# Performance work log

Hardware: AMD Instinct MI355X
Metric: run time of the kernel (lower is better)

## Reference

```python
import jax, jax.numpy as jnp
import numpy as np

N_NODES = 100000
N_EDGES = 1600000
D_IN = 64
D_HID = 64


def setup_inputs() -> dict:
    key = jax.random.key(0)
    ks = jax.random.split(key, 9)
    feat = jax.random.uniform(ks[0], (N_NODES, D_IN), dtype=jnp.float32) + 1e-3
    edge_index = jax.random.randint(ks[1], (2, N_EDGES), 0, N_NODES, dtype=jnp.int64)
    edge_vals = jax.random.uniform(ks[2], (N_EDGES,), dtype=jnp.float32) + 1e-3
    W1 = jax.random.normal(ks[3], (D_IN, D_HID), dtype=jnp.float32) * 0.1
    b1 = jax.random.normal(ks[4], (D_HID,), dtype=jnp.float32) * 0.1
    W2 = jax.random.normal(ks[5], (D_HID, D_HID), dtype=jnp.float32) * 0.1
    b2 = jax.random.normal(ks[6], (D_HID,), dtype=jnp.float32) * 0.1
    W3 = jax.random.normal(ks[7], (D_HID, 1), dtype=jnp.float32) * 0.1
    b3 = jax.random.normal(ks[8], (1,), dtype=jnp.float32) * 0.1
    return {"feat": feat, "edge_index": edge_index, "edge_vals": edge_vals,
            "W1": W1, "b1": b1, "W2": W2, "b2": b2, "W3": W3, "b3": b3}


def reference(feat, edge_index, edge_vals, W1, b1, W2, b2, W3, b3):
    N = feat.shape[0]
    src = edge_index[0]
    dst = edge_index[1]
    # --- __init__: A_hat = D^{-1} A D^{-1}, D = diag(row sums of A) ---
    deg_row = jax.ops.segment_sum(edge_vals, src, num_segments=N)
    deg_row = jnp.where(deg_row > 0, deg_row, 1.0)  # guard isolated nodes
    w_hat = edge_vals / (deg_row[src] * deg_row[dst])  # A_hat edge weights
    # --- GCNConv gcn_norm: add self loops (weight 1), symmetric D^{-1/2} norm ---
    loops = jnp.arange(N, dtype=src.dtype)
    row = jnp.concatenate([src, loops])   # message sources
    col = jnp.concatenate([dst, loops])   # message targets (aggregation index)
    w = jnp.concatenate([w_hat, jnp.ones((N,), dtype=feat.dtype)])
    deg = jax.ops.segment_sum(w, col, num_segments=N)
    dinv = jnp.where(deg > 0, jax.lax.rsqrt(deg), 0.0)
    norm = dinv[row] * w * dinv[col]      # [E+N]

    def gcn_conv(x, W, b):
        h = x @ W                          # [N, d_out]
        msg = norm[:, None] * h[row]       # gather + scale, [E+N, d_out]
        return jax.ops.segment_sum(msg, col, num_segments=N) + b

    # --- forward ---
    x = feat / jnp.sum(feat, axis=1, keepdims=True)
    x = jax.nn.relu(gcn_conv(x, W1, b1))
    x = jax.nn.relu(gcn_conv(x, W2, b2))
    x = gcn_conv(x, W3, b3)               # final layer, no activation
    return x
```

## Files before the change

kernel.cpp:

```cpp
#include <hip/hip_runtime.h>
#include <hip/hip_fp16.h>


#define CAP    48
#define NRL    256
#define NBMX   512
#define P0E    2048

#define PG     2048

__device__ __forceinline__ float dec_ev(unsigned pk) {
    return __half2float(__ushort_as_half((unsigned short)(pk >> 17)));
}
__device__ __forceinline__ float dec_ev15(unsigned pk) {
    return __half2float(__ushort_as_half((unsigned short)(pk & 0x7FFF)));
}

__global__ __launch_bounds__(256) void k_scatter(
        const int* __restrict__ src, const int* __restrict__ dst,
        const float* __restrict__ ev,
        int* __restrict__ meta_d, int2* __restrict__ part_blk,
        int* __restrict__ meta_s, int* __restrict__ parts_src,
        int E, int NB) {
    __shared__ int2 srt[P0E];
    __shared__ int  srs[P0E];
    __shared__ int hd[NBMX], cbd[NBMX], lod[NBMX];
    __shared__ int hs[NBMX], cbs[NBMX], los[NBMX];
    int bx = (int)blockIdx.x, tid = (int)threadIdx.x;
    int e0 = bx * P0E;
    int ne = E - e0; if (ne > P0E) ne = P0E; if (ne < 0) ne = 0;
    for (int i = tid; i < NB; i += 256) { hd[i] = 0; hs[i] = 0; }
    __syncthreads();
    for (int i = tid; i < ne; i += 256) {
        atomicAdd(&hd[dst[e0 + i] >> 8], 1);
        atomicAdd(&hs[src[e0 + i] >> 8], 1);
    }
    __syncthreads();
    int wv = tid >> 6, ln = tid & 63;
    if (wv < 2) {
        int* h  = wv ? hs  : hd;
        int* cb = wv ? cbs : cbd;
        int run = 0;
        #pragma unroll
        for (int k = 0; k < NBMX / 64; k++) {
            int idx = k * 64 + ln;
            int v = (idx < NB) ? h[idx] : 0;
            int sc = v;
            #pragma unroll
            for (int o = 1; o < 64; o <<= 1) {
                int u = __shfl_up(sc, o, 64);
                if (ln >= o) sc += u;
            }
            if (idx < NB) cb[idx] = run + sc - v;
            run += __shfl(sc, 63, 64);
        }
    }
    __syncthreads();
    for (int c = tid; c < NB; c += 256) {
        lod[c] = cbd[c];
        los[c] = cbs[c];
        meta_d[(size_t)bx * NB + c] = (cbd[c] << 16) | hd[c];
        meta_s[(size_t)bx * NB + c] = (cbs[c] << 16) | hs[c];
    }
    __syncthreads();
    for (int i = tid; i < ne; i += 256) {
        int e = e0 + i;
        int s = src[e], d = dst[e];
        float v = ev[e];
        unsigned evh = (unsigned)__half_as_ushort(__float2half_rn(v)) & 0x7FFF;
        int p = atomicAdd(&lod[d >> 8], 1);
        int2 r;
        r.x = ((d & (NRL - 1)) << 17) | s;
        r.y = __float_as_int(v);
        srt[p] = r;
        int q = atomicAdd(&los[s >> 8], 1);
        srs[q] = (int)(((unsigned)(s & (NRL - 1)) << 15) | evh);
    }
    __syncthreads();
    for (int i = tid; i < ne; i += 256) {
        part_blk[(size_t)bx * P0E + i]  = srt[i];
        parts_src[(size_t)bx * P0E + i] = srs[i];
    }
}

__global__ __launch_bounds__(256) void k_degacc(
        const int* __restrict__ parts_src, const int* __restrict__ meta_s,
        float* __restrict__ deg_row, int N, int NB, int nsb) {
    __shared__ float dl[NRL];
    int b = (int)blockIdx.x, tid = (int)threadIdx.x;
    if (tid < NRL) dl[tid] = 0.f;
    __syncthreads();
    for (int bx = tid; bx < nsb; bx += 256) {
        int m = meta_s[(size_t)bx * NB + b];
        int base = m >> 16, len = m & 0xFFFF;
        const int* seg = parts_src + (size_t)bx * P0E + base;
        for (int j = 0; j < len; j++) {
            unsigned pk = (unsigned)seg[j];
            atomicAdd(&dl[pk >> 15], dec_ev15(pk));
        }
    }
    __syncthreads();
    int node = (b << 8) + tid;
    if (tid < NRL && node < N) deg_row[node] = dl[tid];
}

__global__ __launch_bounds__(256) void k_gemm1(
        const float* __restrict__ feat, const float* __restrict__ W1,
        __half* __restrict__ B, int N) {
    int lane = threadIdx.x & 63;
    float w[64];
    #pragma unroll
    for (int k = 0; k < 64; k++) w[k] = W1[k * 64 + lane];
    int wid = (int)blockIdx.x * 4 + (threadIdx.x >> 6);
    const int nw = PG * 4;
    for (int node = wid; node < N; node += nw) {
        float v = feat[(size_t)node * 64 + lane];
        float s = v;
        #pragma unroll
        for (int o = 1; o < 64; o <<= 1) s += __shfl_xor(s, o, 64);
        int myb = __float_as_int(v / s);
        float a0 = 0.f, a1 = 0.f, a2 = 0.f, a3 = 0.f;
        #pragma unroll
        for (int k = 0; k < 64; k += 4) {
            a0 = fmaf(__int_as_float(__builtin_amdgcn_readlane(myb, k + 0)), w[k + 0], a0);
            a1 = fmaf(__int_as_float(__builtin_amdgcn_readlane(myb, k + 1)), w[k + 1], a1);
            a2 = fmaf(__int_as_float(__builtin_amdgcn_readlane(myb, k + 2)), w[k + 2], a2);
            a3 = fmaf(__int_as_float(__builtin_amdgcn_readlane(myb, k + 3)), w[k + 3], a3);
        }
        B[(size_t)node * 64 + lane] = __float2half((a0 + a1) + (a2 + a3));
    }
}

__global__ __launch_bounds__(256) void k_bucket(
        const int2* __restrict__ part_blk, const int* __restrict__ meta_d,
        const float* __restrict__ deg_row,
        int* __restrict__ cnt, int* __restrict__ epair,
        float* __restrict__ di_t, float* __restrict__ r_t,
        int N, int NB, int nsb) {
    __shared__ int   lbuck[NRL * CAP];
    __shared__ int   lcnt[NRL];
    __shared__ float lt[NRL];
    int b = (int)blockIdx.x, tid = (int)threadIdx.x;
    if (tid < NRL) { lcnt[tid] = 0; lt[tid] = 0.f; }
    __syncthreads();
    for (int bx = tid; bx < nsb; bx += 256) {
        int m = meta_d[(size_t)bx * NB + b];
        int base = m >> 16, len = m & 0xFFFF;
        const int2* seg = part_blk + (size_t)bx * P0E + base;
        for (int j = 0; j < len; j++) {
            int2 r = seg[j];
            int dl = (r.x >> 17) & (NRL - 1);
            int s  = r.x & 0x1FFFF;
            float v = __int_as_float(r.y);
            atomicAdd(&lt[dl], v / deg_row[s]);
            unsigned evh = (unsigned)__half_as_ushort(__float2half_rn(v)) & 0x7FFF;
            int p = atomicAdd(&lcnt[dl], 1);
            if (p < CAP) lbuck[dl * CAP + p] = (int)((evh << 17) | (unsigned)s);
        }
    }
    __syncthreads();
    int node0 = b << 8;
    if (tid < NRL) {
        int node = node0 + tid;
        if (node < N) {
            int c = lcnt[tid]; if (c > CAP) c = CAP;
            cnt[node] = c;
            float drd = deg_row[node];
            drd = drd > 0.f ? drd : 1.f;
            float qd = 1.0f / drd;
            float di = rsqrtf(1.0f + qd * lt[tid]);
            di_t[node] = di;
            r_t[node]  = qd * di;
        }
    }
    __syncthreads();
    size_t base = (size_t)node0 * CAP;
    for (int i = tid; i < NRL * CAP; i += 256) epair[base + i] = lbuck[i];
}

__global__ __launch_bounds__(256) void k_p3(const int* __restrict__ cnt,
                                            int* __restrict__ epair,
                                            const float* __restrict__ r_t, int N) {
    int lane = threadIdx.x & 63;
    int node = blockIdx.x * 4 + (threadIdx.x >> 6);
    if (node >= N) return;
    int c = cnt[node]; if (c > CAP) c = CAP;
    if (lane < c) {
        size_t o = (size_t)node * CAP + lane;
        unsigned e = (unsigned)epair[o];
        int s = (int)(e & 0x1FFFF);
        float w = dec_ev(e) * r_t[s];
        unsigned wh = (unsigned)__half_as_ushort(__float2half_rn(w)) & 0x7FFF;
        epair[o] = (int)((wh << 17) | (unsigned)s);
    }
}

__device__ __forceinline__ float gather_rl(int c, int rec,
        const __half* __restrict__ h, int lane) {
    float a0 = 0.f, a1 = 0.f, a2 = 0.f, a3 = 0.f;
    int k = 0;
    for (; k + 16 <= c; k += 16) {
        int e[16]; float hv[16];
        #pragma unroll
        for (int j = 0; j < 16; j++) e[j] = __builtin_amdgcn_readlane(rec, k + j);
        #pragma unroll
        for (int j = 0; j < 16; j++)
            hv[j] = __half2float(h[(size_t)(e[j] & 0x1FFFF) * 64 + lane]);
        #pragma unroll
        for (int j = 0; j < 16; j++) {
            float wv = dec_ev((unsigned)e[j]);
            if ((j & 3) == 0)      a0 = fmaf(wv, hv[j], a0);
            else if ((j & 3) == 1) a1 = fmaf(wv, hv[j], a1);
            else if ((j & 3) == 2) a2 = fmaf(wv, hv[j], a2);
            else                   a3 = fmaf(wv, hv[j], a3);
        }
    }
    for (; k + 8 <= c; k += 8) {
        int e0 = __builtin_amdgcn_readlane(rec, k + 0);
        int e1 = __builtin_amdgcn_readlane(rec, k + 1);
        int e2 = __builtin_amdgcn_readlane(rec, k + 2);
        int e3 = __builtin_amdgcn_readlane(rec, k + 3);
        int e4 = __builtin_amdgcn_readlane(rec, k + 4);
        int e5 = __builtin_amdgcn_readlane(rec, k + 5);
        int e6 = __builtin_amdgcn_readlane(rec, k + 6);
        int e7 = __builtin_amdgcn_readlane(rec, k + 7);
        float h0 = __half2float(h[(size_t)(e0 & 0x1FFFF) * 64 + lane]);
        float h1 = __half2float(h[(size_t)(e1 & 0x1FFFF) * 64 + lane]);
        float h2 = __half2float(h[(size_t)(e2 & 0x1FFFF) * 64 + lane]);
        float h3 = __half2float(h[(size_t)(e3 & 0x1FFFF) * 64 + lane]);
        float h4 = __half2float(h[(size_t)(e4 & 0x1FFFF) * 64 + lane]);
        float h5 = __half2float(h[(size_t)(e5 & 0x1FFFF) * 64 + lane]);
        float h6 = __half2float(h[(size_t)(e6 & 0x1FFFF) * 64 + lane]);
        float h7 = __half2float(h[(size_t)(e7 & 0x1FFFF) * 64 + lane]);
        a0 = fmaf(dec_ev((unsigned)e0), h0, a0);
        a1 = fmaf(dec_ev((unsigned)e1), h1, a1);
        a2 = fmaf(dec_ev((unsigned)e2), h2, a2);
        a3 = fmaf(dec_ev((unsigned)e3), h3, a3);
        a0 = fmaf(dec_ev((unsigned)e4), h4, a0);
        a1 = fmaf(dec_ev((unsigned)e5), h5, a1);
        a2 = fmaf(dec_ev((unsigned)e6), h6, a2);
        a3 = fmaf(dec_ev((unsigned)e7), h7, a3);
    }
    for (; k + 4 <= c; k += 4) {
        int e0 = __builtin_amdgcn_readlane(rec, k + 0);
        int e1 = __builtin_amdgcn_readlane(rec, k + 1);
        int e2 = __builtin_amdgcn_readlane(rec, k + 2);
        int e3 = __builtin_amdgcn_readlane(rec, k + 3);
        float h0 = __half2float(h[(size_t)(e0 & 0x1FFFF) * 64 + lane]);
        float h1 = __half2float(h[(size_t)(e1 & 0x1FFFF) * 64 + lane]);
        float h2 = __half2float(h[(size_t)(e2 & 0x1FFFF) * 64 + lane]);
        float h3 = __half2float(h[(size_t)(e3 & 0x1FFFF) * 64 + lane]);
        a0 = fmaf(dec_ev((unsigned)e0), h0, a0);
        a1 = fmaf(dec_ev((unsigned)e1), h1, a1);
        a2 = fmaf(dec_ev((unsigned)e2), h2, a2);
        a3 = fmaf(dec_ev((unsigned)e3), h3, a3);
    }
    for (; k < c; k++) {
        int e0 = __builtin_amdgcn_readlane(rec, k);
        a0 = fmaf(dec_ev((unsigned)e0),
                  __half2float(h[(size_t)(e0 & 0x1FFFF) * 64 + lane]), a0);
    }
    return (a0 + a1) + (a2 + a3);
}

__global__ __launch_bounds__(256) void k_gath1(
        const int* __restrict__ cnt, const int* __restrict__ epair,
        const __half* __restrict__ B,
        const float* __restrict__ di_t, const float* __restrict__ r_t,
        const float* __restrict__ b1, __half* __restrict__ X2, int N) {
    int lane = threadIdx.x & 63;
    int node = (int)blockIdx.x * 4 + (threadIdx.x >> 6);
    if (node >= N) return;
    int un = __builtin_amdgcn_readfirstlane(node);
    int c  = __builtin_amdgcn_readfirstlane(cnt[un]);
    if (c > CAP) c = CAP;
    int rec = 0;
    if (lane < c) rec = epair[(size_t)un * CAP + lane];
    float own = __half2float(B[(size_t)un * 64 + lane]);
    float g   = gather_rl(c, rec, B, lane);
    float di  = di_t[un], rd = r_t[un];
    float x2  = fmaxf(b1[lane] + di * di * own + rd * g, 0.f);
    X2[(size_t)un * 64 + lane] = __float2half(x2);
}

__global__ __launch_bounds__(256) void k_gemm2(
        const __half* __restrict__ X2, const float* __restrict__ W2,
        __half* __restrict__ C, int N) {
    int lane = threadIdx.x & 63;
    float w[64];
    #pragma unroll
    for (int k = 0; k < 64; k++) w[k] = W2[k * 64 + lane];
    int wid = (int)blockIdx.x * 4 + (threadIdx.x >> 6);
    const int nw = PG * 4;
    for (int node = wid; node < N; node += nw) {
        int myb = __float_as_int(__half2float(X2[(size_t)node * 64 + lane]));
        float a0 = 0.f, a1 = 0.f, a2 = 0.f, a3 = 0.f;
        #pragma unroll
        for (int k = 0; k < 64; k += 4) {
            a0 = fmaf(__int_as_float(__builtin_amdgcn_readlane(myb, k + 0)), w[k + 0], a0);
            a1 = fmaf(__int_as_float(__builtin_amdgcn_readlane(myb, k + 1)), w[k + 1], a1);
            a2 = fmaf(__int_as_float(__builtin_amdgcn_readlane(myb, k + 2)), w[k + 2], a2);
            a3 = fmaf(__int_as_float(__builtin_amdgcn_readlane(myb, k + 3)), w[k + 3], a3);
        }
        C[(size_t)node * 64 + lane] = __float2half((a0 + a1) + (a2 + a3));
    }
}

__global__ __launch_bounds__(256) void k_gather_dot(
        const int* __restrict__ cnt, const int* __restrict__ epair,
        const __half* __restrict__ C,
        const float* __restrict__ di_t, const float* __restrict__ r_t,
        const float* __restrict__ b2, const float* __restrict__ W3,
        float* __restrict__ h3, int N) {
    int lane = threadIdx.x & 63;
    int node = (int)blockIdx.x * 4 + (threadIdx.x >> 6);
    if (node >= N) return;
    int un = __builtin_amdgcn_readfirstlane(node);
    int c  = __builtin_amdgcn_readfirstlane(cnt[un]);
    if (c > CAP) c = CAP;
    int rec = 0;
    if (lane < c) rec = epair[(size_t)un * CAP + lane];
    float own = __half2float(C[(size_t)un * 64 + lane]);
    float g   = gather_rl(c, rec, C, lane);
    float di  = di_t[un], rd = r_t[un];
    float p   = fmaxf(b2[lane] + di * di * own + rd * g, 0.f) * W3[lane];
    #pragma unroll
    for (int o = 1; o < 64; o <<= 1) p += __shfl_xor(p, o, 64);
    if (lane == 0) h3[un] = p;
}

__global__ __launch_bounds__(256) void k_gather1(const int* __restrict__ cnt,
                                                 const int* __restrict__ epair,
                                                 const float* __restrict__ h3,
                                                 const float* __restrict__ di_t,
                                                 const float* __restrict__ r_t,
                                                 const float* __restrict__ b3,
                                                 float* __restrict__ out, int N) {
    int lane = threadIdx.x & 63;
    int node = blockIdx.x * 4 + (threadIdx.x >> 6);
    if (node >= N) return;
    int c = cnt[node]; if (c > CAP) c = CAP;
    float e0 = 0.f;
    if (lane < c) {
        unsigned pk = (unsigned)epair[(size_t)node * CAP + lane];
        e0 = dec_ev(pk) * h3[pk & 0x1FFFF];
    }
    #pragma unroll
    for (int o = 1; o < 64; o <<= 1) e0 += __shfl_xor(e0, o, 64);
    if (lane == 0) {
        float di = di_t[node];
        out[node] = b3[0] + di * di * h3[node] + r_t[node] * e0;
    }
}

extern "C" void kernel_launch(void* const* d_in, const int* in_sizes, int n_in,
                              void* d_out, int out_size, void* d_ws, size_t ws_size,
                              hipStream_t stream) {
    const float* feat = (const float*)d_in[0];
    const int*   eidx = (const int*)d_in[1];
    const float* ev   = (const float*)d_in[2];
    const float* W1 = (const float*)d_in[3];
    const float* b1 = (const float*)d_in[4];
    const float* W2 = (const float*)d_in[5];
    const float* b2 = (const float*)d_in[6];
    const float* W3 = (const float*)d_in[7];
    const float* b3 = (const float*)d_in[8];

    const int N = in_sizes[0] / 64;
    const int E = in_sizes[2];
    const int* src = eidx;
    const int* dst = eidx + E;
    const int NB   = (N + NRL - 1) / NRL;
    const int npad = NB * NRL;
    const int nsb  = (E + P0E - 1) / P0E;

    char* p = (char*)d_ws;
    auto carve = [&](size_t nbytes) { char* r = p; p += (nbytes + 255) & ~(size_t)255; return r; };
    float*    deg_row   = (float*)   carve((size_t)N * 4);
    float*    di_t      = (float*)   carve((size_t)N * 4);
    float*    r_t       = (float*)   carve((size_t)N * 4);
    float*    h3        = (float*)   carve((size_t)N * 4);
    int*      cnt       = (int*)     carve((size_t)npad * 4);
    int*      meta_d    = (int*)     carve((size_t)nsb * NB * 4);
    int*      meta_s    = (int*)     carve((size_t)nsb * NB * 4);
    int*      epair     = (int*)     carve((size_t)npad * CAP * 4);
    int2*     part_blk  = (int2*)    carve((size_t)nsb * P0E * 8);
    int*      parts_src = (int*)     carve((size_t)nsb * P0E * 4);
    __half*   B         = (__half*)  carve((size_t)N * 64 * 2);
    __half*   X2        = (__half*)part_blk;
    __half*   C         = (__half*)B;
    float*    out       = (float*)d_out;

    const int BLK = 256;
    int gNode4 = (N + 3) / 4;

    k_scatter   <<<nsb, BLK, 0, stream>>>(src, dst, ev, meta_d, part_blk,
                                          meta_s, parts_src, E, NB);
    k_degacc    <<<NB, BLK, 0, stream>>>(parts_src, meta_s, deg_row, N, NB, nsb);
    k_gemm1     <<<PG, BLK, 0, stream>>>(feat, W1, B, N);
    k_bucket    <<<NB, BLK, 0, stream>>>(part_blk, meta_d, deg_row, cnt, epair,
                                         di_t, r_t, N, NB, nsb);
    k_p3        <<<gNode4, BLK, 0, stream>>>(cnt, epair, r_t, N);

    k_gath1     <<<gNode4, BLK, 0, stream>>>(cnt, epair, B, di_t, r_t, b1, X2, N);
    k_gemm2     <<<PG, BLK, 0, stream>>>(X2, W2, C, N);
    k_gather_dot<<<gNode4, BLK, 0, stream>>>(cnt, epair, C, di_t, r_t,
                                             b2, W3, h3, N);
    k_gather1   <<<gNode4, BLK, 0, stream>>>(cnt, epair, h3, di_t, r_t, b3, out, N);
}
```

Before: 330.5 us.

## Gather 8 neighbor rows per wave with 16-byte vector loads

Replaces the per-lane scalar half loads in the neighbor gather with a scheme where the wave is split into 8 groups of 8 lanes. Each group fetches a different neighbor's 128-byte feature row using uint4 loads, accumulates 8 features per lane, and then reduces across groups with xor shuffles. This aims to cut the number of memory instructions and increase memory-level parallelism on the random-access gather. In exchange it adds a cross-group shuffle reduction, leaves partially idle lanes when degree is not a multiple of 8, and changes the order of float accumulation.

```diff
diff --git a/kernel.cpp b/kernel.cpp
--- a/kernel.cpp
+++ b/kernel.cpp
@@ -195,72 +195,49 @@
     }
 }
 
-__device__ __forceinline__ float gather_rl(int c, int rec,
-        const __half* __restrict__ h, int lane) {
-    float a0 = 0.f, a1 = 0.f, a2 = 0.f, a3 = 0.f;
-    int k = 0;
-    for (; k + 16 <= c; k += 16) {
-        int e[16]; float hv[16];
+__device__ __forceinline__ void gather8(int c, int rec,
+        const __half* __restrict__ h, int grp, int sub, float acc[8]) {
+    #pragma unroll
+    for (int q = 0; q < 8; q++) acc[q] = 0.f;
+    int nb = (c + 7) >> 3;
+    for (int t = 0; t < nb; t += 2) {
+        int r0 = __shfl(rec, (t << 3) + grp, 64);
+        int s0 = r0 & 0x1FFFF;
+        float w0 = dec_ev((unsigned)r0);
+        uint4 d0 = *reinterpret_cast<const uint4*>(h + ((size_t)s0 << 6) + (sub << 3));
+        bool have1 = (t + 1 < nb);
+        uint4 d1; float w1 = 0.f;
+        if (have1) {
+            int r1 = __shfl(rec, (t << 3) + 8 + grp, 64);
+            int s1 = r1 & 0x1FFFF;
+            w1 = dec_ev((unsigned)r1);
+            d1 = *reinterpret_cast<const uint4*>(h + ((size_t)s1 << 6) + (sub << 3));
+        }
+        {
+            const __half2* p0 = reinterpret_cast<const __half2*>(&d0);
+            #pragma unroll
+            for (int q = 0; q < 4; q++) {
+                float2 f = __half22float2(p0[q]);
+                acc[2 * q]     = fmaf(w0, f.x, acc[2 * q]);
+                acc[2 * q + 1] = fmaf(w0, f.y, acc[2 * q + 1]);
+            }
+        }
+        if (have1) {
+            const __half2* p1 = reinterpret_cast<const __half2*>(&d1);
+            #pragma unroll
+            for (int q = 0; q < 4; q++) {
+                float2 f = __half22float2(p1[q]);
+                acc[2 * q]     = fmaf(w1, f.x, acc[2 * q]);
+                acc[2 * q + 1] = fmaf(w1, f.y, acc[2 * q + 1]);
+            }
+        }
+    }
+    #pragma unroll
+    for (int o = 8; o < 64; o <<= 1) {
         #pragma unroll
-        for (int j = 0; j < 16; j++) e[j] = __builtin_amdgcn_readlane(rec, k + j);
-        #pragma unroll
-        for (int j = 0; j < 16; j++)
-            hv[j] = __half2float(h[(size_t)(e[j] & 0x1FFFF) * 64 + lane]);
-        #pragma unroll
-        for (int j = 0; j < 16; j++) {
-            float wv = dec_ev((unsigned)e[j]);
-            if ((j & 3) == 0)      a0 = fmaf(wv, hv[j], a0);
-            else if ((j & 3) == 1) a1 = fmaf(wv, hv[j], a1);
-            else if ((j & 3) == 2) a2 = fmaf(wv, hv[j], a2);
-            else                   a3 = fmaf(wv, hv[j], a3);
-        }
-    }
-    for (; k + 8 <= c; k += 8) {
-        int e0 = __builtin_amdgcn_readlane(rec, k + 0);
-        int e1 = __builtin_amdgcn_readlane(rec, k + 1);
-        int e2 = __builtin_amdgcn_readlane(rec, k + 2);
-        int e3 = __builtin_amdgcn_readlane(rec, k + 3);
-        int e4 = __builtin_amdgcn_readlane(rec, k + 4);
-        int e5 = __builtin_amdgcn_readlane(rec, k + 5);
-        int e6 = __builtin_amdgcn_readlane(rec, k + 6);
-        int e7 = __builtin_amdgcn_readlane(rec, k + 7);
-        float h0 = __half2float(h[(size_t)(e0 & 0x1FFFF) * 64 + lane]);
-        float h1 = __half2float(h[(size_t)(e1 & 0x1FFFF) * 64 + lane]);
-        float h2 = __half2float(h[(size_t)(e2 & 0x1FFFF) * 64 + lane]);
-        float h3 = __half2float(h[(size_t)(e3 & 0x1FFFF) * 64 + lane]);
-        float h4 = __half2float(h[(size_t)(e4 & 0x1FFFF) * 64 + lane]);
-        float h5 = __half2float(h[(size_t)(e5 & 0x1FFFF) * 64 + lane]);
-        float h6 = __half2float(h[(size_t)(e6 & 0x1FFFF) * 64 + lane]);
-        float h7 = __half2float(h[(size_t)(e7 & 0x1FFFF) * 64 + lane]);
-        a0 = fmaf(dec_ev((unsigned)e0), h0, a0);
-        a1 = fmaf(dec_ev((unsigned)e1), h1, a1);
-        a2 = fmaf(dec_ev((unsigned)e2), h2, a2);
-        a3 = fmaf(dec_ev((unsigned)e3), h3, a3);
-        a0 = fmaf(dec_ev((unsigned)e4), h4, a0);
-        a1 = fmaf(dec_ev((unsigned)e5), h5, a1);
-        a2 = fmaf(dec_ev((unsigned)e6), h6, a2);
-        a3 = fmaf(dec_ev((unsigned)e7), h7, a3);
-    }
-    for (; k + 4 <= c; k += 4) {
-        int e0 = __builtin_amdgcn_readlane(rec, k + 0);
-        int e1 = __builtin_amdgcn_readlane(rec, k + 1);
-        int e2 = __builtin_amdgcn_readlane(rec, k + 2);
-        int e3 = __builtin_amdgcn_readlane(rec, k + 3);
-        float h0 = __half2float(h[(size_t)(e0 & 0x1FFFF) * 64 + lane]);
-        float h1 = __half2float(h[(size_t)(e1 & 0x1FFFF) * 64 + lane]);
-        float h2 = __half2float(h[(size_t)(e2 & 0x1FFFF) * 64 + lane]);
-        float h3 = __half2float(h[(size_t)(e3 & 0x1FFFF) * 64 + lane]);
-        a0 = fmaf(dec_ev((unsigned)e0), h0, a0);
-        a1 = fmaf(dec_ev((unsigned)e1), h1, a1);
-        a2 = fmaf(dec_ev((unsigned)e2), h2, a2);
-        a3 = fmaf(dec_ev((unsigned)e3), h3, a3);
-    }
-    for (; k < c; k++) {
-        int e0 = __builtin_amdgcn_readlane(rec, k);
-        a0 = fmaf(dec_ev((unsigned)e0),
-                  __half2float(h[(size_t)(e0 & 0x1FFFF) * 64 + lane]), a0);
-    }
-    return (a0 + a1) + (a2 + a3);
+        for (int q = 0; q < 8; q++)
+            acc[q] += __shfl_xor(acc[q], o, 64);
+    }
 }
 
 __global__ __launch_bounds__(256) void k_gath1(
@@ -269,6 +246,7 @@
         const float* __restrict__ di_t, const float* __restrict__ r_t,
         const float* __restrict__ b1, __half* __restrict__ X2, int N) {
     int lane = threadIdx.x & 63;
+    int grp = lane >> 3, sub = lane & 7;
     int node = (int)blockIdx.x * 4 + (threadIdx.x >> 6);
     if (node >= N) return;
     int un = __builtin_amdgcn_readfirstlane(node);
@@ -276,11 +254,36 @@
     if (c > CAP) c = CAP;
     int rec = 0;
     if (lane < c) rec = epair[(size_t)un * CAP + lane];
-    float own = __half2float(B[(size_t)un * 64 + lane]);
-    float g   = gather_rl(c, rec, B, lane);
-    float di  = di_t[un], rd = r_t[un];
-    float x2  = fmaxf(b1[lane] + di * di * own + rd * g, 0.f);
-    X2[(size_t)un * 64 + lane] = __float2half(x2);
+    uint4 dow = *reinterpret_cast<const uint4*>(B + ((size_t)un << 6) + (sub << 3));
+    float g[8];
+    gather8(c, rec, B, grp, sub, g);
+    float di = di_t[un], rd = r_t[un];
+    float dd = di * di;
+    const float4* b4 = reinterpret_cast<const float4*>(b1);
+    float4 bA = b4[sub * 2], bB = b4[sub * 2 + 1];
+    const __half2* po = reinterpret_cast<const __half2*>(&dow);
+    float2 o0 = __half22float2(po[0]), o1 = __half22float2(po[1]);
+    float2 o2 = __half22float2(po[2]), o3 = __half22float2(po[3]);
+    float x0 = fmaxf(bA.x + dd * o0.x + rd * g[0], 0.f);
+    float x1 = fmaxf(bA.y + dd * o0.y + rd * g[1], 0.f);
+    float x2 = fmaxf(bA.z + dd * o1.x + rd * g[2], 0.f);
+    float x3 = fmaxf(bA.w + dd * o1.y + rd * g[3], 0.f);
+    float x4 = fmaxf(bB.x + dd * o2.x + rd * g[4], 0.f);
+    float x5 = fmaxf(bB.y + dd * o2.y + rd * g[5], 0.f);
+    float x6 = fmaxf(bB.z + dd * o3.x + rd * g[6], 0.f);
+    float x7 = fmaxf(bB.w + dd * o3.y + rd * g[7], 0.f);
+    if (grp == 0) {
+        __half2 h0 = __floats2half2_rn(x0, x1);
+        __half2 h1 = __floats2half2_rn(x2, x3);
+        __half2 h2 = __floats2half2_rn(x4, x5);
+        __half2 h3 = __floats2half2_rn(x6, x7);
+        uint4 ov;
+        ov.x = *reinterpret_cast<unsigned*>(&h0);
+        ov.y = *reinterpret_cast<unsigned*>(&h1);
+        ov.z = *reinterpret_cast<unsigned*>(&h2);
+        ov.w = *reinterpret_cast<unsigned*>(&h3);
+        *reinterpret_cast<uint4*>(X2 + ((size_t)un << 6) + (sub << 3)) = ov;
+    }
 }
 
 __global__ __launch_bounds__(256) void k_gemm2(
@@ -313,6 +316,7 @@
         const float* __restrict__ b2, const float* __restrict__ W3,
         float* __restrict__ h3, int N) {
     int lane = threadIdx.x & 63;
+    int grp = lane >> 3, sub = lane & 7;
     int node = (int)blockIdx.x * 4 + (threadIdx.x >> 6);
     if (node >= N) return;
     int un = __builtin_amdgcn_readfirstlane(node);
@@ -320,13 +324,30 @@
     if (c > CAP) c = CAP;
     int rec = 0;
     if (lane < c) rec = epair[(size_t)un * CAP + lane];
-    float own = __half2float(C[(size_t)un * 64 + lane]);
-    float g   = gather_rl(c, rec, C, lane);
-    float di  = di_t[un], rd = r_t[un];
-    float p   = fmaxf(b2[lane] + di * di * own + rd * g, 0.f) * W3[lane];
-    #pragma unroll
-    for (int o = 1; o < 64; o <<= 1) p += __shfl_xor(p, o, 64);
-    if (lane == 0) h3[un] = p;
+    uint4 dow = *reinterpret_cast<const uint4*>(C + ((size_t)un << 6) + (sub << 3));
+    float g[8];
+    gather8(c, rec, C, grp, sub, g);
+    float di = di_t[un], rd = r_t[un];
+    float dd = di * di;
+    const float4* b4 = reinterpret_cast<const float4*>(b2);
+    const float4* w4 = reinterpret_cast<const float4*>(W3);
+    float4 bA = b4[sub * 2], bB = b4[sub * 2 + 1];
+    float4 wA = w4[sub * 2], wB = w4[sub * 2 + 1];
+    const __half2* po = reinterpret_cast<const __half2*>(&dow);
+    float2 o0 = __half22float2(po[0]), o1 = __half22float2(po[1]);
+    float2 o2 = __half22float2(po[2]), o3 = __half22float2(po[3]);
+    float pd = 0.f;
+    pd += fmaxf(bA.x + dd * o0.x + rd * g[0], 0.f) * wA.x;
+    pd += fmaxf(bA.y + dd * o0.y + rd * g[1], 0.f) * wA.y;
+    pd += fmaxf(bA.z + dd * o1.x + rd * g[2], 0.f) * wA.z;
+    pd += fmaxf(bA.w + dd * o1.y + rd * g[3], 0.f) * wA.w;
+    pd += fmaxf(bB.x + dd * o2.x + rd * g[4], 0.f) * wB.x;
+    pd += fmaxf(bB.y + dd * o2.y + rd * g[5], 0.f) * wB.y;
+    pd += fmaxf(bB.z + dd * o3.x + rd * g[6], 0.f) * wB.z;
+    pd += fmaxf(bB.w + dd * o3.y + rd * g[7], 0.f) * wB.w;
+    #pragma unroll
+    for (int o = 1; o < 8; o <<= 1) pd += __shfl_xor(pd, o, 64);
+    if (lane == 0) h3[un] = pd;
 }
 
 __global__ __launch_bounds__(256) void k_gather1(const int* __restrict__ cnt,
```

After: 327.9 us. No clear change (-0.8%).
